# Kernel optimization log

Hardware: AMD Instinct MI355X
Metric: run time of the kernel (lower is better)

Reference implementation:

```python
import jax, jax.numpy as jnp
import numpy as np
import math

EMBED_DIM = 2048
NUM_Q_HEADS = 32
NUM_KV_HEADS = 8
HEAD_DIM = EMBED_DIM // NUM_Q_HEADS  # 64
GROUP = NUM_Q_HEADS // NUM_KV_HEADS  # 4
THETA = 10000.0


def _rope_tables(T, D):
    # matches torch.polar(ones, outer(pos, inv_freq)) -> cos/sin of shape (T, D//2)
    dim_half = D // 2
    inv_freq = 1.0 / (THETA ** (jnp.arange(dim_half, dtype=jnp.float32) / dim_half))
    freqs = jnp.arange(T, dtype=jnp.float32)[:, None] * inv_freq[None, :]  # (T, D//2)
    return jnp.cos(freqs), jnp.sin(freqs)


def _apply_rope(x, cos, sin):
    # x: (B, H, T, D); interleaved complex pairs along last dim, as in view_as_complex
    B, H, T, D = x.shape
    xp = x.reshape(B, H, T, D // 2, 2)
    xr, xi = xp[..., 0], xp[..., 1]
    c = cos[None, None, :, :]
    s = sin[None, None, :, :]
    or_ = xr * c - xi * s
    oi_ = xr * s + xi * c
    return jnp.stack([or_, oi_], axis=-1).reshape(B, H, T, D)


def setup_inputs() -> dict:
    key = jax.random.key(0)
    ks = jax.random.split(key, 5)
    B, T, C = 2, 2048, EMBED_DIM
    kvC = NUM_KV_HEADS * HEAD_DIM
    x = jax.random.normal(ks[0], (B, T, C), dtype=jnp.float32)
    Wq = jax.random.normal(ks[1], (C, C), dtype=jnp.float32) * 0.02
    Wk = jax.random.normal(ks[2], (kvC, C), dtype=jnp.float32) * 0.02
    Wv = jax.random.normal(ks[3], (kvC, C), dtype=jnp.float32) * 0.02
    Wo = jax.random.normal(ks[4], (C, C), dtype=jnp.float32) * 0.02
    return {"x": x, "Wq": Wq, "Wk": Wk, "Wv": Wv, "Wo": Wo}


def reference(x, Wq, Wk, Wv, Wo):
    B, T, C = x.shape
    Hq, Hkv, D, G = NUM_Q_HEADS, NUM_KV_HEADS, HEAD_DIM, GROUP
    scale = 1.0 / math.sqrt(D)

    q = (x @ Wq.T).reshape(B, T, Hq, D).transpose(0, 2, 1, 3)   # (B,Hq,T,D)
    k = (x @ Wk.T).reshape(B, T, Hkv, D).transpose(0, 2, 1, 3)  # (B,Hkv,T,D)
    v = (x @ Wv.T).reshape(B, T, Hkv, D).transpose(0, 2, 1, 3)

    cos, sin = _rope_tables(T, D)
    q = _apply_rope(q, cos, sin)
    k = _apply_rope(k, cos, sin)  # RoPE commutes with head repeat; same math

    # grouped attention: avoid materializing repeat_interleave of K/V
    qg = q.reshape(B, Hkv, G, T, D)
    att = jnp.einsum("bhgtd,bhsd->bhgts", qg, k) * scale  # (B,Hkv,G,T,T)

    causal = jnp.tril(jnp.ones((T, T), dtype=bool))
    att = jnp.where(causal[None, None, None, :, :], att, -jnp.inf)
    att = jax.nn.softmax(att, axis=-1)
    # dropout is identity in eval mode

    out = jnp.einsum("bhgts,bhsd->bhgtd", att, v)  # (B,Hkv,G,T,D)
    out = out.reshape(B, Hq, T, D).transpose(0, 2, 1, 3).reshape(B, T, C)
    return out @ Wo.T
```

## Files before the change

kernel.cpp:

```cpp
#include <hip/hip_runtime.h>
#include <hip/hip_bf16.h>
#include <math.h>

#define T_SEQ 2048
#define BATCH 2
#define CDIM  2048
#define HQ    32
#define HKV   8
#define HD    64
#define GRP   4
#define NQKV  3072

typedef __attribute__((ext_vector_type(8))) short  bf16x8;
typedef __attribute__((ext_vector_type(8))) ushort u16x8;
typedef __attribute__((ext_vector_type(4))) float  f32x4;

static __device__ __forceinline__ float bf2f(ushort u) {
    union { unsigned int ui; float f; } v; v.ui = ((unsigned int)u) << 16; return v.f;
}
static __device__ __forceinline__ ushort f2bf(float f) {
    union { float f; unsigned int ui; } v; v.f = f;
    unsigned int r = v.ui + 0x7FFFu + ((v.ui >> 16) & 1u);
    return (ushort)(r >> 16);
}
static __device__ __forceinline__ unsigned int pack2bf(float a, float b) {
    __hip_bfloat162 h = __float22bfloat162_rn(float2{a, b});
    union { __hip_bfloat162 h; unsigned int u; } v; v.h = h; return v.u;
}

__global__ void cvt5_kernel(const float* __restrict__ x,  const float* __restrict__ wq,
                            const float* __restrict__ wk, const float* __restrict__ wv,
                            const float* __restrict__ wo,
                            ushort* __restrict__ xb, ushort* __restrict__ wqkvb,
                            ushort* __restrict__ wob) {
    long c = (long)blockIdx.x * blockDim.x + threadIdx.x;
    const float* src; ushort* dst; long off;
    if (c < 1048576L)      { src = x;  dst = xb;              off = c; }
    else if (c < 1572864L) { src = wq; dst = wqkvb;           off = c - 1048576L; }
    else if (c < 1703936L) { src = wk; dst = wqkvb + 4194304; off = c - 1572864L; }
    else if (c < 1835008L) { src = wv; dst = wqkvb + 5242880; off = c - 1703936L; }
    else                   { src = wo; dst = wob;             off = c - 1835008L; }
    long i = off * 8;
    float4 a = *(const float4*)(src + i);
    float4 b = *(const float4*)(src + i + 4);
    u16x8 v;
    v[0] = f2bf(a.x); v[1] = f2bf(a.y); v[2] = f2bf(a.z); v[3] = f2bf(a.w);
    v[4] = f2bf(b.x); v[5] = f2bf(b.y); v[6] = f2bf(b.z); v[7] = f2bf(b.w);
    *(u16x8*)(dst + i) = v;
}

template<bool F32OUT>
__global__ __launch_bounds__(256) void gemm_bt(const ushort* __restrict__ A,
                                               const ushort* __restrict__ B,
                                               void* __restrict__ C,
                                               int M, int N, int K) {
    __shared__ ushort As[2][128 * 64];
    __shared__ ushort Bs[2][128 * 64];
    const int tid  = threadIdx.x;
    const int wave = tid >> 6;
    const int lane = tid & 63;

    const int nbx = gridDim.x;
    int wg = blockIdx.y * nbx + blockIdx.x;
    const int nwg = nbx * gridDim.y;
    const int cpx = nwg >> 3;
    wg = (wg & 7) * cpx + (wg >> 3);
    const int bm = wg % nbx, bn = wg / nbx;
    const int wm = wave >> 1, wn = wave & 1;

    f32x4 acc[4][4];
    #pragma unroll
    for (int i = 0; i < 4; ++i)
        #pragma unroll
        for (int j = 0; j < 4; ++j) { acc[i][j][0]=0.f; acc[i][j][1]=0.f; acc[i][j][2]=0.f; acc[i][j][3]=0.f; }

    const int r_sub = tid >> 3;
    const int c_src = (((tid & 7) ^ (r_sub & 7))) * 8;
    const int lr = lane & 15, lg = lane >> 4;

    const int nkt = K >> 6;

    auto STAGE = [&](int k0, int db) {
        #pragma unroll
        for (int it = 0; it < 4; ++it) {
            int row = it * 32 + r_sub;
            const ushort* srcA = A + (size_t)(bm * 128 + row) * K + k0 + c_src;
            const ushort* srcB = B + (size_t)(bn * 128 + row) * K + k0 + c_src;
            __builtin_amdgcn_global_load_lds(
                (const __attribute__((address_space(1))) unsigned int*)srcA,
                (__attribute__((address_space(3))) unsigned int*)((char*)&As[db][0] + it * 4096 + wave * 1024),
                16, 0, 0);
            __builtin_amdgcn_global_load_lds(
                (const __attribute__((address_space(1))) unsigned int*)srcB,
                (__attribute__((address_space(3))) unsigned int*)((char*)&Bs[db][0] + it * 4096 + wave * 1024),
                16, 0, 0);
        }
    };

    STAGE(0, 0);
    __syncthreads();

    for (int t = 0; t < nkt; ++t) {
        const int db = t & 1;
        if (t + 1 < nkt) STAGE((t + 1) << 6, db ^ 1);

        #pragma unroll
        for (int kk = 0; kk < 2; ++kk) {
            bf16x8 af[4], bfr[4];
            #pragma unroll
            for (int mi = 0; mi < 4; ++mi)
                af[mi] = *(const bf16x8*)&As[db][(wm * 64 + mi * 16 + lr) * 64 + (((kk * 4 + lg) ^ (lr & 7)) * 8)];
            #pragma unroll
            for (int ni = 0; ni < 4; ++ni)
                bfr[ni] = *(const bf16x8*)&Bs[db][(wn * 64 + ni * 16 + lr) * 64 + (((kk * 4 + lg) ^ (lr & 7)) * 8)];
            __builtin_amdgcn_s_setprio(1);
            #pragma unroll
            for (int mi = 0; mi < 4; ++mi)
                #pragma unroll
                for (int ni = 0; ni < 4; ++ni)
                    acc[mi][ni] = __builtin_amdgcn_mfma_f32_16x16x32_bf16(af[mi], bfr[ni], acc[mi][ni], 0, 0, 0);
            __builtin_amdgcn_s_setprio(0);
        }
        __syncthreads();
    }

    #pragma unroll
    for (int mi = 0; mi < 4; ++mi)
        #pragma unroll
        for (int ni = 0; ni < 4; ++ni)
            #pragma unroll
            for (int r = 0; r < 4; ++r) {
                int row = bm * 128 + wm * 64 + mi * 16 + lg * 4 + r;
                int col = bn * 128 + wn * 64 + ni * 16 + lr;
                float v = acc[mi][ni][r];
                if (F32OUT) ((float*)C)[(size_t)row * N + col] = v;
                else        ((ushort*)C)[(size_t)row * N + col] = f2bf(v);
            }
}

__global__ void rope_qk(const ushort* __restrict__ qkv, ushort* __restrict__ Qh, ushort* __restrict__ Kh) {
    const int NQP = BATCH * T_SEQ * HQ * (HD / 2);
    int i = blockIdx.x * blockDim.x + threadIdx.x;
    if (i < NQP) {
        int row = i >> 10;
        int idx = i & 1023;
        int h = idx >> 5, j = idx & 31;
        int t = row & (T_SEQ - 1), b = row >> 11;
        const ushort* src = qkv + (size_t)row * NQKV + h * HD + 2 * j;
        unsigned int pin = *(const unsigned int*)src;
        float xr = bf2f((ushort)(pin & 0xFFFF));
        float xi = bf2f((ushort)(pin >> 16));
        float ang = (float)t * exp2f((float)j * -0.4152410118609203f);
        float c, s; sincosf(ang, &s, &c);
        float orr = xr * c - xi * s;
        float oi  = xr * s + xi * c;
        unsigned int pout = (unsigned int)f2bf(orr) | ((unsigned int)f2bf(oi) << 16);
        ushort* dst = Qh + ((size_t)((b * HQ + h) * T_SEQ + t)) * HD + 2 * j;
        *(unsigned int*)dst = pout;
    } else {
        int ii = i - NQP;
        int row = ii >> 8;
        int idx = ii & 255;
        int hk = idx >> 5, j = idx & 31;
        int t = row & (T_SEQ - 1), b = row >> 11;
        const ushort* src = qkv + (size_t)row * NQKV + CDIM + hk * HD + 2 * j;
        unsigned int pin = *(const unsigned int*)src;
        float xr = bf2f((ushort)(pin & 0xFFFF));
        float xi = bf2f((ushort)(pin >> 16));
        float ang = (float)t * exp2f((float)j * -0.4152410118609203f);
        float c, s; sincosf(ang, &s, &c);
        float orr = xr * c - xi * s;
        float oi  = xr * s + xi * c;
        unsigned int pout = (unsigned int)f2bf(orr) | ((unsigned int)f2bf(oi) << 16);
        ushort* dst = Kh + ((size_t)((b * HKV + hk) * T_SEQ + t)) * HD + 2 * j;
        *(unsigned int*)dst = pout;
    }
}

__global__ __launch_bounds__(256) void v_transpose(const ushort* __restrict__ qkv, ushort* __restrict__ Vt) {
    __shared__ ushort Vs[64][80];
    int bh = blockIdx.x;
    int tt = blockIdx.y;
    int b = bh >> 3, hk = bh & 7;
    int tid = threadIdx.x;
    #pragma unroll
    for (int c = 0; c < 2; ++c) {
        int rr = tid + c * 256;
        int tl = rr >> 3, d0 = (rr & 7) * 8;
        int row = b * T_SEQ + tt * 64 + tl;
        u16x8 v = *(const u16x8*)(qkv + (size_t)row * NQKV + CDIM + HKV * HD + hk * HD + d0);
        *(u16x8*)&Vs[tl][d0] = v;
    }
    __syncthreads();
    #pragma unroll
    for (int c = 0; c < 2; ++c) {
        int ch = tid + c * 256;
        int d = ch >> 3, t8 = (ch & 7) * 8;
        u16x8 o;
        #pragma unroll
        for (int j = 0; j < 8; ++j) o[j] = Vs[t8 + j][d];
        *(u16x8*)(Vt + ((size_t)(bh * HD + d)) * T_SEQ + tt * 64 + t8) = o;
    }
}

__global__ __launch_bounds__(256) void attn_kernel(const ushort* __restrict__ Qh,
                                                   const ushort* __restrict__ Kh,
                                                   const ushort* __restrict__ Vt,
                                                   ushort* __restrict__ O) {
    __shared__ ushort Ks[2][64 * 64];
    __shared__ ushort Vs[2][64 * 64];
    __shared__ ushort Ps[4][16 * 64];
    const int pairi = blockIdx.x, h = blockIdx.y, b = blockIdx.z;
    const int hk = h >> 2;
    const int tid = threadIdx.x, wave = tid >> 6, lane = tid & 63;
    const int lr = lane & 15, lg = lane >> 4;
    const float CEXP = 0.1803368801111204f;

    const ushort* Kbase = Kh + (size_t)(b * HKV + hk) * T_SEQ * HD;
    const ushort* Vbase = Vt + (size_t)(b * HKV + hk) * HD * T_SEQ;
    const int srow = tid >> 3, scol = (tid & 7) * 8;
    const int psw = (lr ^ (lr >> 3)) & 7;

    bf16x8 onesf;
    #pragma unroll
    for (int j = 0; j < 8; ++j) onesf[j] = (short)0x3F80;

    #pragma unroll
    for (int phalf = 0; phalf < 2; ++phalf) {
        const int qb = phalf ? (31 - pairi) : pairi;
        const ushort* Qbase = Qh + ((size_t)((b * HQ + h) * T_SEQ + qb * 64 + wave * 16 + lr)) * HD;
        bf16x8 qf[2];
        qf[0] = *(const bf16x8*)(Qbase + lg * 8);
        qf[1] = *(const bf16x8*)(Qbase + 32 + lg * 8);

        f32x4 oacc[4];
        #pragma unroll
        for (int dt = 0; dt < 4; ++dt) { oacc[dt][0]=0.f; oacc[dt][1]=0.f; oacc[dt][2]=0.f; oacc[dt][3]=0.f; }
        float l_r[4];
        #pragma unroll
        for (int r = 0; r < 4; ++r) l_r[r] = 0.f;
        float m_run = -INFINITY;

        const int q_glob = qb * 64 + wave * 16 + lr;
        const int nkt = qb + 1;

        u16x8 rK[2], rV[2];
        #pragma unroll
        for (int hh = 0; hh < 2; ++hh) {
            int r0 = srow + hh * 32;
            rK[hh] = *(const u16x8*)(Kbase + (size_t)r0 * HD + scol);
            rV[hh] = *(const u16x8*)(Vbase + (size_t)r0 * T_SEQ + scol);
        }
        __syncthreads();

        for (int kt = 0; kt < nkt; ++kt) {
            const int t0 = kt * 64;
            const int buf = kt & 1;
            #pragma unroll
            for (int hh = 0; hh < 2; ++hh) {
                int r0 = srow + hh * 32;
                int cb = (((tid & 7) ^ (r0 & 7))) * 8;
                *(u16x8*)&Ks[buf][r0 * 64 + cb] = rK[hh];
                *(u16x8*)&Vs[buf][r0 * 64 + cb] = rV[hh];
            }
            if (kt + 1 < nkt) {
                const int t1 = t0 + 64;
                #pragma unroll
                for (int hh = 0; hh < 2; ++hh) {
                    int r0 = srow + hh * 32;
                    rK[hh] = *(const u16x8*)(Kbase + (size_t)(t1 + r0) * HD + scol);
                    rV[hh] = *(const u16x8*)(Vbase + (size_t)r0 * T_SEQ + t1 + scol);
                }
            }
            __syncthreads();

            f32x4 sacc[4];
            #pragma unroll
            for (int ct = 0; ct < 4; ++ct) { sacc[ct][0]=0.f; sacc[ct][1]=0.f; sacc[ct][2]=0.f; sacc[ct][3]=0.f; }
            __builtin_amdgcn_s_setprio(1);
            #pragma unroll
            for (int kk = 0; kk < 2; ++kk) {
                #pragma unroll
                for (int ct = 0; ct < 4; ++ct) {
                    bf16x8 kf = *(const bf16x8*)&Ks[buf][(ct * 16 + lr) * 64 + (((kk * 4 + lg) ^ (lr & 7)) * 8)];
                    sacc[ct] = __builtin_amdgcn_mfma_f32_16x16x32_bf16(kf, qf[kk], sacc[ct], 0, 0, 0);
                }
            }
            __builtin_amdgcn_s_setprio(0);

            if (kt == qb) {
                #pragma unroll
                for (int ct = 0; ct < 4; ++ct) {
                    #pragma unroll
                    for (int r = 0; r < 4; ++r) {
                        int k_glob = t0 + ct * 16 + lg * 4 + r;
                        if (k_glob > q_glob) sacc[ct][r] = -INFINITY;
                    }
                }
            }

            float pm = sacc[0][0];
            #pragma unroll
            for (int ct = 0; ct < 4; ++ct)
                #pragma unroll
                for (int r = 0; r < 4; ++r) pm = fmaxf(pm, sacc[ct][r]);
            pm = fmaxf(pm, __shfl_xor(pm, 16));
            pm = fmaxf(pm, __shfl_xor(pm, 32));

            bool cskip = (pm <= m_run + 64.f);
            if (!__all(cskip)) {
                float mn = fmaxf(m_run, pm);
                float al = exp2f(CEXP * (m_run - mn));
                m_run = mn;
                #pragma unroll
                for (int r = 0; r < 4; ++r) {
                    float alq = __shfl(al, lg * 4 + r);
                    l_r[r] *= alq;
                    #pragma unroll
                    for (int dt = 0; dt < 4; ++dt) oacc[dt][r] *= alq;
                }
            }

            const float cm = CEXP * m_run;
            #pragma unroll
            for (int ct = 0; ct < 4; ++ct) {
                float p0 = exp2f(fmaf(CEXP, sacc[ct][0], -cm));
                float p1 = exp2f(fmaf(CEXP, sacc[ct][1], -cm));
                float p2 = exp2f(fmaf(CEXP, sacc[ct][2], -cm));
                float p3 = exp2f(fmaf(CEXP, sacc[ct][3], -cm));
                uint2 w; w.x = pack2bf(p0, p1); w.y = pack2bf(p2, p3);
                *(uint2*)&Ps[wave][lr * 64 + (((ct * 2 + (lg >> 1)) ^ psw) * 8) + (lg & 1) * 4] = w;
            }

            f32x4 lacc;
            lacc[0]=0.f; lacc[1]=0.f; lacc[2]=0.f; lacc[3]=0.f;
            __builtin_amdgcn_s_setprio(1);
            #pragma unroll
            for (int kk = 0; kk < 2; ++kk) {
                bf16x8 pf = *(const bf16x8*)&Ps[wave][lr * 64 + (((kk * 4 + lg) ^ psw) * 8)];
                lacc = __builtin_amdgcn_mfma_f32_16x16x32_bf16(pf, onesf, lacc, 0, 0, 0);
                #pragma unroll
                for (int dt = 0; dt < 4; ++dt) {
                    bf16x8 vf = *(const bf16x8*)&Vs[buf][(dt * 16 + lr) * 64 + (((kk * 4 + lg) ^ (lr & 7)) * 8)];
                    oacc[dt] = __builtin_amdgcn_mfma_f32_16x16x32_bf16(pf, vf, oacc[dt], 0, 0, 0);
                }
            }
            __builtin_amdgcn_s_setprio(0);
            #pragma unroll
            for (int r = 0; r < 4; ++r) l_r[r] += lacc[r];
        }

        #pragma unroll
        for (int dt = 0; dt < 4; ++dt)
            #pragma unroll
            for (int r = 0; r < 4; ++r) {
                int t = qb * 64 + wave * 16 + lg * 4 + r;
                int d = dt * 16 + lr;
                float v = oacc[dt][r] / l_r[r];
                O[((size_t)(b * T_SEQ + t)) * CDIM + h * HD + d] = f2bf(v);
            }
    }
}

extern "C" void kernel_launch(void* const* d_in, const int* in_sizes, int n_in,
                              void* d_out, int out_size, void* d_ws, size_t ws_size,
                              hipStream_t stream) {
    const float* x  = (const float*)d_in[0];
    const float* Wq = (const float*)d_in[1];
    const float* Wk = (const float*)d_in[2];
    const float* Wv = (const float*)d_in[3];
    const float* Wo = (const float*)d_in[4];
    float* out = (float*)d_out;

    ushort* xb    = (ushort*)d_ws;
    ushort* wqkvb = xb    + 8388608;
    ushort* wob   = wqkvb + 6291456;
    ushort* qkv   = wob   + 4194304;
    ushort* Qh    = qkv   + 12582912;
    ushort* Kh    = Qh    + 8388608;
    ushort* Vt    = Kh    + 2097152;
    ushort* attO  = xb;

    cvt5_kernel<<<9216, 256, 0, stream>>>(x, Wq, Wk, Wv, Wo, xb, wqkvb, wob);

    gemm_bt<false><<<dim3(32, 24), 256, 0, stream>>>(xb, wqkvb, qkv, 4096, 3072, 2048);

    rope_qk<<<20480, 256, 0, stream>>>(qkv, Qh, Kh);
    v_transpose<<<dim3(16, 32), 256, 0, stream>>>(qkv, Vt);

    attn_kernel<<<dim3(16, 32, 2), 256, 0, stream>>>(Qh, Kh, Vt, attO);

    gemm_bt<true><<<dim3(32, 16), 256, 0, stream>>>(attO, wob, out, 4096, 2048, 2048);
}
```

Baseline: 323.1 us.

## Widen attention blocks to 128 query rows with 8 waves sharing K/V tiles

The attention kernel now runs 512 threads (8 waves) per block, each block covering 128 query rows instead of 64. The grid is halved, and each K/V tile staged in shared memory is reused by twice as many waves, which cuts global K/V loads and the per-thread staging work. Waves whose rows lie entirely before a key tile skip its compute via a per-wave causal check. They still hit the barriers, so some waves idle on the diagonal tiles. The change also hoists swizzled LDS address math and swaps the final division for a reciprocal multiply.

```diff
diff --git a/kernel.cpp b/kernel.cpp
--- a/kernel.cpp
+++ b/kernel.cpp
@@ -203,13 +203,13 @@
     }
 }
 
-__global__ __launch_bounds__(256) void attn_kernel(const ushort* __restrict__ Qh,
+__global__ __launch_bounds__(512) void attn_kernel(const ushort* __restrict__ Qh,
                                                    const ushort* __restrict__ Kh,
                                                    const ushort* __restrict__ Vt,
                                                    ushort* __restrict__ O) {
     __shared__ ushort Ks[2][64 * 64];
     __shared__ ushort Vs[2][64 * 64];
-    __shared__ ushort Ps[4][16 * 64];
+    __shared__ ushort Ps[8][16 * 64];
     const int pairi = blockIdx.x, h = blockIdx.y, b = blockIdx.z;
     const int hk = h >> 2;
     const int tid = threadIdx.x, wave = tid >> 6, lane = tid & 63;
@@ -221,14 +221,25 @@
     const int srow = tid >> 3, scol = (tid & 7) * 8;
     const int psw = (lr ^ (lr >> 3)) & 7;
 
+    const int swofs = srow * 64 + (((tid & 7) ^ (srow & 7)) * 8);
+    ushort* const kw0 = &Ks[0][swofs]; ushort* const kw1 = &Ks[1][swofs];
+    ushort* const vw0 = &Vs[0][swofs]; ushort* const vw1 = &Vs[1][swofs];
+    int rdk[2];
+    #pragma unroll
+    for (int kk = 0; kk < 2; ++kk) rdk[kk] = (((kk * 4 + lg) ^ (lr & 7)) * 8);
+    const int lr64 = lr * 64;
+    int prk[2];
+    #pragma unroll
+    for (int kk = 0; kk < 2; ++kk) prk[kk] = lr64 + (((kk * 4 + lg) ^ psw) * 8);
+
     bf16x8 onesf;
     #pragma unroll
     for (int j = 0; j < 8; ++j) onesf[j] = (short)0x3F80;
 
     #pragma unroll
     for (int phalf = 0; phalf < 2; ++phalf) {
-        const int qb = phalf ? (31 - pairi) : pairi;
-        const ushort* Qbase = Qh + ((size_t)((b * HQ + h) * T_SEQ + qb * 64 + wave * 16 + lr)) * HD;
+        const int qb = phalf ? (15 - pairi) : pairi;
+        const ushort* Qbase = Qh + ((size_t)((b * HQ + h) * T_SEQ + qb * 128 + wave * 16 + lr)) * HD;
         bf16x8 qf[2];
         qf[0] = *(const bf16x8*)(Qbase + lg * 8);
         qf[1] = *(const bf16x8*)(Qbase + 32 + lg * 8);
@@ -241,122 +252,120 @@
         for (int r = 0; r < 4; ++r) l_r[r] = 0.f;
         float m_run = -INFINITY;
 
-        const int q_glob = qb * 64 + wave * 16 + lr;
-        const int nkt = qb + 1;
-
-        u16x8 rK[2], rV[2];
-        #pragma unroll
-        for (int hh = 0; hh < 2; ++hh) {
-            int r0 = srow + hh * 32;
-            rK[hh] = *(const u16x8*)(Kbase + (size_t)r0 * HD + scol);
-            rV[hh] = *(const u16x8*)(Vbase + (size_t)r0 * T_SEQ + scol);
-        }
+        const int q0w = qb * 128 + wave * 16;
+        const int q_glob = q0w + lr;
+        const int nkt = 2 * qb + 2;
+
+        const ushort* kp = Kbase + (size_t)srow * HD + scol;
+        const ushort* vp = Vbase + (size_t)srow * T_SEQ + scol;
+        u16x8 rK = *(const u16x8*)kp;
+        u16x8 rV = *(const u16x8*)vp;
+        kp += 64 * HD; vp += 64;
         __syncthreads();
 
         for (int kt = 0; kt < nkt; ++kt) {
             const int t0 = kt * 64;
             const int buf = kt & 1;
-            #pragma unroll
-            for (int hh = 0; hh < 2; ++hh) {
-                int r0 = srow + hh * 32;
-                int cb = (((tid & 7) ^ (r0 & 7))) * 8;
-                *(u16x8*)&Ks[buf][r0 * 64 + cb] = rK[hh];
-                *(u16x8*)&Vs[buf][r0 * 64 + cb] = rV[hh];
-            }
+            *(u16x8*)(buf ? kw1 : kw0) = rK;
+            *(u16x8*)(buf ? vw1 : vw0) = rV;
             if (kt + 1 < nkt) {
-                const int t1 = t0 + 64;
-                #pragma unroll
-                for (int hh = 0; hh < 2; ++hh) {
-                    int r0 = srow + hh * 32;
-                    rK[hh] = *(const u16x8*)(Kbase + (size_t)(t1 + r0) * HD + scol);
-                    rV[hh] = *(const u16x8*)(Vbase + (size_t)r0 * T_SEQ + t1 + scol);
-                }
+                rK = *(const u16x8*)kp;
+                rV = *(const u16x8*)vp;
+                kp += 64 * HD; vp += 64;
             }
             __syncthreads();
 
-            f32x4 sacc[4];
-            #pragma unroll
-            for (int ct = 0; ct < 4; ++ct) { sacc[ct][0]=0.f; sacc[ct][1]=0.f; sacc[ct][2]=0.f; sacc[ct][3]=0.f; }
-            __builtin_amdgcn_s_setprio(1);
-            #pragma unroll
-            for (int kk = 0; kk < 2; ++kk) {
-                #pragma unroll
-                for (int ct = 0; ct < 4; ++ct) {
-                    bf16x8 kf = *(const bf16x8*)&Ks[buf][(ct * 16 + lr) * 64 + (((kk * 4 + lg) ^ (lr & 7)) * 8)];
-                    sacc[ct] = __builtin_amdgcn_mfma_f32_16x16x32_bf16(kf, qf[kk], sacc[ct], 0, 0, 0);
+            if (t0 <= q0w + 15) {
+                const ushort* ksb = buf ? &Ks[1][0] : &Ks[0][0];
+                const ushort* vsb = buf ? &Vs[1][0] : &Vs[0][0];
+
+                f32x4 sacc[4];
+                #pragma unroll
+                for (int ct = 0; ct < 4; ++ct) { sacc[ct][0]=0.f; sacc[ct][1]=0.f; sacc[ct][2]=0.f; sacc[ct][3]=0.f; }
+                __builtin_amdgcn_s_setprio(1);
+                #pragma unroll
+                for (int kk = 0; kk < 2; ++kk) {
+                    #pragma unroll
+                    for (int ct = 0; ct < 4; ++ct) {
+                        bf16x8 kf = *(const bf16x8*)&ksb[(ct * 16 + lr) * 64 + rdk[kk]];
+                        sacc[ct] = __builtin_amdgcn_mfma_f32_16x16x32_bf16(kf, qf[kk], sacc[ct], 0, 0, 0);
+                    }
                 }
-            }
-            __builtin_amdgcn_s_setprio(0);
-
-            if (kt == qb) {
-                #pragma unroll
-                for (int ct = 0; ct < 4; ++ct) {
+                __builtin_amdgcn_s_setprio(0);
+
+                if (t0 + 63 > q0w) {
+                    #pragma unroll
+                    for (int ct = 0; ct < 4; ++ct) {
+                        #pragma unroll
+                        for (int r = 0; r < 4; ++r) {
+                            int k_glob = t0 + ct * 16 + lg * 4 + r;
+                            if (k_glob > q_glob) sacc[ct][r] = -INFINITY;
+                        }
+                    }
+                }
+
+                float pm = sacc[0][0];
+                #pragma unroll
+                for (int ct = 0; ct < 4; ++ct)
+                    #pragma unroll
+                    for (int r = 0; r < 4; ++r) pm = fmaxf(pm, sacc[ct][r]);
+                pm = fmaxf(pm, __shfl_xor(pm, 16));
+                pm = fmaxf(pm, __shfl_xor(pm, 32));
+
+                bool cskip = (pm <= m_run + 64.f);
+                if (!__all(cskip)) {
+                    float mn = fmaxf(m_run, pm);
+                    float al = exp2f(CEXP * (m_run - mn));
+                    m_run = mn;
                     #pragma unroll
                     for (int r = 0; r < 4; ++r) {
-                        int k_glob = t0 + ct * 16 + lg * 4 + r;
-                        if (k_glob > q_glob) sacc[ct][r] = -INFINITY;
+                        float alq = __shfl(al, lg * 4 + r);
+                        l_r[r] *= alq;
+                        #pragma unroll
+                        for (int dt = 0; dt < 4; ++dt) oacc[dt][r] *= alq;
                     }
                 }
+
+                const float cm = CEXP * m_run;
+                #pragma unroll
+                for (int ct = 0; ct < 4; ++ct) {
+                    float p0 = exp2f(fmaf(CEXP, sacc[ct][0], -cm));
+                    float p1 = exp2f(fmaf(CEXP, sacc[ct][1], -cm));
+                    float p2 = exp2f(fmaf(CEXP, sacc[ct][2], -cm));
+                    float p3 = exp2f(fmaf(CEXP, sacc[ct][3], -cm));
+                    uint2 w; w.x = pack2bf(p0, p1); w.y = pack2bf(p2, p3);
+                    *(uint2*)&Ps[wave][lr64 + (((ct * 2 + (lg >> 1)) ^ psw) * 8) + (lg & 1) * 4] = w;
+                }
+
+                f32x4 lacc;
+                lacc[0]=0.f; lacc[1]=0.f; lacc[2]=0.f; lacc[3]=0.f;
+                __builtin_amdgcn_s_setprio(1);
+                #pragma unroll
+                for (int kk = 0; kk < 2; ++kk) {
+                    bf16x8 pf = *(const bf16x8*)&Ps[wave][prk[kk]];
+                    lacc = __builtin_amdgcn_mfma_f32_16x16x32_bf16(pf, onesf, lacc, 0, 0, 0);
+                    #pragma unroll
+                    for (int dt = 0; dt < 4; ++dt) {
+                        bf16x8 vf = *(const bf16x8*)&vsb[(dt * 16 + lr) * 64 + rdk[kk]];
+                        oacc[dt] = __builtin_amdgcn_mfma_f32_16x16x32_bf16(pf, vf, oacc[dt], 0, 0, 0);
+                    }
+                }
+                __builtin_amdgcn_s_setprio(0);
+                #pragma unroll
+                for (int r = 0; r < 4; ++r) l_r[r] += lacc[r];
             }
-
-            float pm = sacc[0][0];
-            #pragma unroll
-            for (int ct = 0; ct < 4; ++ct)
-                #pragma unroll
-                for (int r = 0; r < 4; ++r) pm = fmaxf(pm, sacc[ct][r]);
-            pm = fmaxf(pm, __shfl_xor(pm, 16));
-            pm = fmaxf(pm, __shfl_xor(pm, 32));
-
-            bool cskip = (pm <= m_run + 64.f);
-            if (!__all(cskip)) {
-                float mn = fmaxf(m_run, pm);
-                float al = exp2f(CEXP * (m_run - mn));
-                m_run = mn;
-                #pragma unroll
-                for (int r = 0; r < 4; ++r) {
-                    float alq = __shfl(al, lg * 4 + r);
-                    l_r[r] *= alq;
-                    #pragma unroll
-                    for (int dt = 0; dt < 4; ++dt) oacc[dt][r] *= alq;
-                }
-            }
-
-            const float cm = CEXP * m_run;
-            #pragma unroll
-            for (int ct = 0; ct < 4; ++ct) {
-                float p0 = exp2f(fmaf(CEXP, sacc[ct][0], -cm));
-                float p1 = exp2f(fmaf(CEXP, sacc[ct][1], -cm));
-                float p2 = exp2f(fmaf(CEXP, sacc[ct][2], -cm));
-                float p3 = exp2f(fmaf(CEXP, sacc[ct][3], -cm));
-                uint2 w; w.x = pack2bf(p0, p1); w.y = pack2bf(p2, p3);
-                *(uint2*)&Ps[wave][lr * 64 + (((ct * 2 + (lg >> 1)) ^ psw) * 8) + (lg & 1) * 4] = w;
-            }
-
-            f32x4 lacc;
-            lacc[0]=0.f; lacc[1]=0.f; lacc[2]=0.f; lacc[3]=0.f;
-            __builtin_amdgcn_s_setprio(1);
-            #pragma unroll
-            for (int kk = 0; kk < 2; ++kk) {
-                bf16x8 pf = *(const bf16x8*)&Ps[wave][lr * 64 + (((kk * 4 + lg) ^ psw) * 8)];
-                lacc = __builtin_amdgcn_mfma_f32_16x16x32_bf16(pf, onesf, lacc, 0, 0, 0);
-                #pragma unroll
-                for (int dt = 0; dt < 4; ++dt) {
-                    bf16x8 vf = *(const bf16x8*)&Vs[buf][(dt * 16 + lr) * 64 + (((kk * 4 + lg) ^ (lr & 7)) * 8)];
-                    oacc[dt] = __builtin_amdgcn_mfma_f32_16x16x32_bf16(pf, vf, oacc[dt], 0, 0, 0);
-                }
-            }
-            __builtin_amdgcn_s_setprio(0);
-            #pragma unroll
-            for (int r = 0; r < 4; ++r) l_r[r] += lacc[r];
         }
 
+        float linv[4];
+        #pragma unroll
+        for (int r = 0; r < 4; ++r) linv[r] = 1.0f / l_r[r];
         #pragma unroll
         for (int dt = 0; dt < 4; ++dt)
             #pragma unroll
             for (int r = 0; r < 4; ++r) {
-                int t = qb * 64 + wave * 16 + lg * 4 + r;
+                int t = qb * 128 + wave * 16 + lg * 4 + r;
                 int d = dt * 16 + lr;
-                float v = oacc[dt][r] / l_r[r];
+                float v = oacc[dt][r] * linv[r];
                 O[((size_t)(b * T_SEQ + t)) * CDIM + h * HD + d] = f2bf(v);
             }
     }
@@ -388,7 +397,7 @@
     rope_qk<<<20480, 256, 0, stream>>>(qkv, Qh, Kh);
     v_transpose<<<dim3(16, 32), 256, 0, stream>>>(qkv, Vt);
 
-    attn_kernel<<<dim3(16, 32, 2), 256, 0, stream>>>(Qh, Kh, Vt, attO);
+    attn_kernel<<<dim3(8, 32, 2), 512, 0, stream>>>(Qh, Kh, Vt, attO);
 
     gemm_bt<true><<<dim3(32, 16), 256, 0, stream>>>(attO, wob, out, 4096, 2048, 2048);
 }
```

After: 306.1 us. 5.3% less time.
